# Kernel tuning notes

Measured on AMD Instinct MI355X. Metric: run time of the kernel, lower is better.

## Reference

```python
import jax, jax.numpy as jnp
import numpy as np

EPSILON = 1e-36


def setup_inputs() -> dict:
    key = jax.random.key(0)
    k1, k2, k3, k4 = jax.random.split(key, 4)
    n, in_dim, out_dim = 8192, 128, 128
    x = jax.random.normal(k1, (n, in_dim), dtype=jnp.float32)
    # xavier-uniform-like scale for W_real
    limit = float(np.sqrt(6.0 / (in_dim + out_dim)))
    W_real = jax.random.uniform(k2, (in_dim, out_dim), dtype=jnp.float32, minval=-limit, maxval=limit)
    W_imag = jax.random.uniform(k3, (in_dim, out_dim), dtype=jnp.float32, minval=-0.1, maxval=0.1)
    G = jax.random.uniform(k4, (in_dim, out_dim), dtype=jnp.float32, minval=0.0, maxval=1.0)
    return {"x": x, "W_real": W_real, "W_imag": W_imag, "G": G}


def reference(x, W_real, W_imag, G):
    Gc = jnp.clip(G, 0.0, 1.0)                                   # (i,o)
    # R: (n,i,o) = |x| gated toward 1 by (1-G)
    R = (jnp.abs(x) + EPSILON)[:, :, None] * Gc[None] + (1.0 - Gc)[None]
    # K: pi where x<0, gated by G
    K = jnp.pi * (x < 0).astype(x.dtype)[:, :, None] * Gc[None]  # (n,i,o)
    logR = jnp.log(R)
    A = jnp.einsum('nio,io->no', logR, W_real) - jnp.einsum('nio,io->no', K, W_imag)
    B = jnp.einsum('nio,io->no', logR, W_imag) + jnp.einsum('nio,io->no', K, W_real)
    return jnp.exp(A) * jnp.cos(B)
```

## Files before the change

kernel.cpp:

```cpp
#include <hip/hip_runtime.h>
#include <math.h>


#define NROWS 8192
#define DIM   128
#define RPB   8
#define NT    512
#define IQ    32
#define PI_F  3.14159265358979323846f
#define LN2_F 0.69314718055994530942f

typedef float v2f __attribute__((ext_vector_type(2)));

static __device__ __forceinline__ v2f vfma2(v2f a, v2f b, v2f c) {
    return __builtin_elementwise_fma(a, b, c);
}

__global__ __launch_bounds__(NT, 4) void main_kernel(
    const float* __restrict__ x,
    const float* __restrict__ Wr, const float* __restrict__ Wi,
    const float* __restrict__ G, float* __restrict__ out)
{
    __shared__ float sbuf[4 * RPB * DIM];
    float* am1p = sbuf;
    float* psp  = sbuf + DIM * RPB;

    const int tid   = threadIdx.x;
    const int o     = tid & (DIM - 1);
    const int q     = tid >> 7;
    const int nbase = blockIdx.x * RPB;

    {
        const float* xb = x + (size_t)nbase * DIM;
        float2 v = ((const float2*)xb)[tid];
        int e = tid * 2;
        int i = e & (DIM - 1), r = e >> 7;
        am1p[i * RPB + r]       = fabsf(v.x) - 1.0f;
        am1p[(i + 1) * RPB + r] = fabsf(v.y) - 1.0f;
        psp[i * RPB + r]        = (v.x < 0.0f) ? PI_F : 0.0f;
        psp[(i + 1) * RPB + r]  = (v.y < 0.0f) ? PI_F : 0.0f;
    }
    __syncthreads();

    v2f accA[4], accB[4];
#pragma unroll
    for (int p = 0; p < 4; ++p) { accA[p] = (v2f){0.f, 0.f}; accB[p] = (v2f){0.f, 0.f}; }

    const int ibase = q * IQ;
    const int wo    = ibase * DIM + o;

#pragma unroll 4
    for (int ii = 0; ii < IQ; ++ii) {
        const int i  = ibase + ii;
        const int wi_idx = wo + ii * DIM;

        float g   = fminf(fmaxf(G[wi_idx], 0.0f), 1.0f);
        float wrl = LN2_F * Wr[wi_idx];
        float wil = LN2_F * Wi[wi_idx];

        const float ngwi = -g * (wil * (1.0f / LN2_F));
        const float gwr  =  g * (wrl * (1.0f / LN2_F));
        const v2f gg2   = {g, g};
        const v2f wrl2  = {wrl, wrl};
        const v2f wil2  = {wil, wil};
        const v2f ngwi2 = {ngwi, ngwi};
        const v2f gwr2  = {gwr, gwr};
        const v2f one2  = {1.0f, 1.0f};

        const float4* a4 = (const float4*)(am1p + i * RPB);
        const float4* p4 = (const float4*)(psp  + i * RPB);
        float4 a03 = a4[0], a47 = a4[1];
        float4 s03 = p4[0], s47 = p4[1];

#define ROWPAIR(mx, my, sx, sy, idx)                                        \
        do {                                                                \
            v2f t2 = vfma2((v2f){mx, my}, gg2, one2);                       \
            v2f l2 = { __log2f(t2.x), __log2f(t2.y) };                      \
            v2f s2 = {sx, sy};                                              \
            accA[idx] = vfma2(l2, wrl2, vfma2(s2, ngwi2, accA[idx]));       \
            accB[idx] = vfma2(l2, wil2, vfma2(s2, gwr2,  accB[idx]));       \
        } while (0)

        ROWPAIR(a03.x, a03.y, s03.x, s03.y, 0);
        ROWPAIR(a03.z, a03.w, s03.z, s03.w, 1);
        ROWPAIR(a47.x, a47.y, s47.x, s47.y, 2);
        ROWPAIR(a47.z, a47.w, s47.z, s47.w, 3);
#undef ROWPAIR
    }

    float* pP = sbuf;
    const int c = tid * 2;
    const int r = c >> 7, oo = c & (DIM - 1);

    __syncthreads();
#pragma unroll
    for (int p = 0; p < 4; ++p) {
        pP[q * (RPB * DIM) + (2 * p) * DIM + o]     = accA[p].x;
        pP[q * (RPB * DIM) + (2 * p + 1) * DIM + o] = accA[p].y;
    }
    __syncthreads();
    v2f A = {0.f, 0.f};
#pragma unroll
    for (int qq = 0; qq < 4; ++qq)
        A += *(const v2f*)&pP[qq * (RPB * DIM) + r * DIM + oo];
    __syncthreads();
#pragma unroll
    for (int p = 0; p < 4; ++p) {
        pP[q * (RPB * DIM) + (2 * p) * DIM + o]     = accB[p].x;
        pP[q * (RPB * DIM) + (2 * p + 1) * DIM + o] = accB[p].y;
    }
    __syncthreads();
    v2f B = {0.f, 0.f};
#pragma unroll
    for (int qq = 0; qq < 4; ++qq)
        B += *(const v2f*)&pP[qq * (RPB * DIM) + r * DIM + oo];

    float2 res;
    res.x = __expf(A.x) * __cosf(B.x);
    res.y = __expf(A.y) * __cosf(B.y);
    *(float2*)&out[(size_t)(nbase + r) * DIM + oo] = res;
}

extern "C" void kernel_launch(void* const* d_in, const int* in_sizes, int n_in,
                              void* d_out, int out_size, void* d_ws, size_t ws_size,
                              hipStream_t stream) {
    const float* x  = (const float*)d_in[0];
    const float* Wr = (const float*)d_in[1];
    const float* Wi = (const float*)d_in[2];
    const float* G  = (const float*)d_in[3];
    float* out = (float*)d_out;

    (void)d_ws; (void)ws_size;

    main_kernel<<<NROWS / RPB, NT, 0, stream>>>(x, Wr, Wi, G, out);
}
```

Baseline: 88.55 us.

## Precompute gated weight terms in a prep kernel and broadcast x via readlane

A small prep kernel folds the clip, the LN2 scaling and the pi*G*W products into packed float4/float2 weight arrays in workspace. The main kernel then does one log per (row,i) shared across both A and B outputs by packing A and B into a v2f, reads x values via readlane instead of LDS staging, and software-prefetches the next weight row. It also raises the occupancy hint and falls back to the old kernel when workspace is too small. This trades an extra launch and larger weight reads for fewer per-element ALU ops.

```diff
diff --git a/kernel.cpp b/kernel.cpp
--- a/kernel.cpp
+++ b/kernel.cpp
@@ -6,7 +6,6 @@
 #define DIM   128
 #define RPB   8
 #define NT    512
-#define IQ    32
 #define PI_F  3.14159265358979323846f
 #define LN2_F 0.69314718055994530942f
 
@@ -16,7 +15,98 @@
     return __builtin_elementwise_fma(a, b, c);
 }
 
-__global__ __launch_bounds__(NT, 4) void main_kernel(
+__global__ __launch_bounds__(256) void prep(
+    const float* __restrict__ Wr, const float* __restrict__ Wi,
+    const float* __restrict__ G,
+    float4* __restrict__ wq, float2* __restrict__ wb)
+{
+    int t = blockIdx.x * 256 + threadIdx.x;
+    if (t < DIM * DIM) {
+        float g  = fminf(fmaxf(G[t], 0.0f), 1.0f);
+        float wr = Wr[t], wi = Wi[t];
+        wq[t] = make_float4(LN2_F * wr, LN2_F * wi, g, 1.0f - g);
+        wb[t] = make_float2(-PI_F * g * wi, PI_F * g * wr);
+    }
+}
+
+__global__ __launch_bounds__(NT, 8) void main_kernel(
+    const float* __restrict__ x, const float4* __restrict__ wq,
+    const float2* __restrict__ wb, float* __restrict__ out)
+{
+    __shared__ float2 P[8][RPB][64];
+
+    const int tid   = threadIdx.x;
+    const int lane  = tid & 63;
+    const int w     = tid >> 6;
+    const int h     = w & 1;
+    const int iq    = w >> 1;
+    const int i0    = iq * 32;
+    const int nbase = blockIdx.x * RPB;
+    const int o     = h * 64 + lane;
+
+    float vx[4];
+#pragma unroll
+    for (int k = 0; k < 4; ++k)
+        vx[k] = x[(size_t)(nbase + 2 * k + (lane >> 5)) * DIM + i0 + (lane & 31)];
+
+    v2f acc[RPB];
+#pragma unroll
+    for (int r = 0; r < RPB; ++r) acc[r] = (v2f){0.f, 0.f};
+
+    const float4* wqp = wq + (size_t)i0 * DIM + o;
+    const float2* wbp = wb + (size_t)i0 * DIM + o;
+
+    float4 wqc = wqp[0];
+    float2 wbc = wbp[0];
+
+#pragma unroll 2
+    for (int ii = 0; ii < 32; ++ii) {
+        const int nx = (ii + 1) & 31;
+        float4 wqn = wqp[(size_t)nx * DIM];
+        float2 wbn = wbp[(size_t)nx * DIM];
+
+        const float g  = wqc.z;
+        const float hh = wqc.w;
+        const v2f   w2  = {wqc.x, wqc.y};
+        const v2f   pg2 = {wbc.x, wbc.y};
+
+#pragma unroll
+        for (int r = 0; r < RPB; ++r) {
+            int   xi = __builtin_amdgcn_readlane(__float_as_int(vx[r >> 1]),
+                                                 (r & 1) * 32 + ii);
+            float xr = __int_as_float(xi);
+            float ax = fabsf(xr);
+            float sf = (xr < 0.0f) ? 1.0f : 0.0f;
+            float t  = fmaf(g, ax, hh);
+            float l  = __log2f(t);
+            acc[r] = vfma2((v2f){l, l}, w2,
+                           vfma2((v2f){sf, sf}, pg2, acc[r]));
+        }
+        wqc = wqn; wbc = wbn;
+    }
+
+#pragma unroll
+    for (int r = 0; r < RPB; ++r)
+        P[w][r][lane] = make_float2(acc[r].x, acc[r].y);
+    __syncthreads();
+
+#pragma unroll
+    for (int cc = 0; cc < 2; ++cc) {
+        const int c  = tid + cc * NT;
+        const int r  = c >> 7;
+        const int oo = c & (DIM - 1);
+        const int h2 = oo >> 6, ol = oo & 63;
+        float A = 0.f, B = 0.f;
+#pragma unroll
+        for (int q2 = 0; q2 < 4; ++q2) {
+            float2 p = P[q2 * 2 + h2][r][ol];
+            A += p.x; B += p.y;
+        }
+        out[(size_t)(nbase + r) * DIM + oo] = __expf(A) * __cosf(B);
+    }
+}
+
+__global__ __launch_bounds__(NT, 4) void fb_kernel(
     const float* __restrict__ x,
     const float* __restrict__ Wr, const float* __restrict__ Wi,
     const float* __restrict__ G, float* __restrict__ out)
@@ -46,26 +136,18 @@
 #pragma unroll
     for (int p = 0; p < 4; ++p) { accA[p] = (v2f){0.f, 0.f}; accB[p] = (v2f){0.f, 0.f}; }
 
-    const int ibase = q * IQ;
-    const int wo    = ibase * DIM + o;
-
+    const int ibase = q * 32;
 #pragma unroll 4
-    for (int ii = 0; ii < IQ; ++ii) {
-        const int i  = ibase + ii;
-        const int wi_idx = wo + ii * DIM;
-
+    for (int ii = 0; ii < 32; ++ii) {
+        const int i = ibase + ii;
+        const int wi_idx = i * DIM + o;
         float g   = fminf(fmaxf(G[wi_idx], 0.0f), 1.0f);
         float wrl = LN2_F * Wr[wi_idx];
         float wil = LN2_F * Wi[wi_idx];
-
         const float ngwi = -g * (wil * (1.0f / LN2_F));
         const float gwr  =  g * (wrl * (1.0f / LN2_F));
-        const v2f gg2   = {g, g};
-        const v2f wrl2  = {wrl, wrl};
-        const v2f wil2  = {wil, wil};
-        const v2f ngwi2 = {ngwi, ngwi};
-        const v2f gwr2  = {gwr, gwr};
-        const v2f one2  = {1.0f, 1.0f};
+        const v2f gg2 = {g, g}, wrl2 = {wrl, wrl}, wil2 = {wil, wil};
+        const v2f ngwi2 = {ngwi, ngwi}, gwr2 = {gwr, gwr}, one2 = {1.f, 1.f};
 
         const float4* a4 = (const float4*)(am1p + i * RPB);
         const float4* p4 = (const float4*)(psp  + i * RPB);
@@ -130,7 +212,14 @@
     const float* G  = (const float*)d_in[3];
     float* out = (float*)d_out;
 
-    (void)d_ws; (void)ws_size;
-
-    main_kernel<<<NROWS / RPB, NT, 0, stream>>>(x, Wr, Wi, G, out);
-}
+    const size_t wq_bytes = (size_t)DIM * DIM * sizeof(float4);
+    const size_t wb_bytes = (size_t)DIM * DIM * sizeof(float2);
+    if (ws_size >= wq_bytes + wb_bytes) {
+        float4* wq = (float4*)d_ws;
+        float2* wb = (float2*)((char*)d_ws + wq_bytes);
+        prep<<<(DIM * DIM + 255) / 256, 256, 0, stream>>>(Wr, Wi, G, wq, wb);
+        main_kernel<<<NROWS / RPB, NT, 0, stream>>>(x, wq, wb, out);
+    } else {
+        fb_kernel<<<NROWS / RPB, NT, 0, stream>>>(x, Wr, Wi, G, out);
+    }
+}
```

Measured after the change: 98.79 us. 1.12x slower.
